# Performance work log

Measured on AMD Instinct MI355X. Metric: run time of the kernel, lower is better.

The kernel has to match this reference:

```python
import jax, jax.numpy as jnp
import numpy as np


def phi(x):
    # ELU + 1 feature map (Katharopoulos et al. 2020)
    return jax.nn.elu(x) + 1.0


def setup_inputs() -> dict:
    key = jax.random.key(0)
    k1, k2, k3 = jax.random.split(key, 3)
    B, T, D = 2, 2048, 512
    x = jax.random.normal(k1, (B, T, D), dtype=jnp.float32)
    # torch nn.Linear stores weight as (out_features, in_features)
    w_qkv = jax.random.normal(k2, (3 * D, D), dtype=jnp.float32) * 0.02
    w_out = jax.random.normal(k3, (D, D), dtype=jnp.float32) * 0.02
    return {"x": x, "w_qkv": w_qkv, "w_out": w_out, "n_heads": 16}


def reference(x, w_qkv, w_out, n_heads):
    B, T, D = x.shape
    H = n_heads
    Dh = D // H
    qkv = x @ w_qkv.T                                   # (B,T,3D)
    qkv = qkv.reshape(B, T, 3, H, Dh).transpose(2, 0, 3, 1, 4)  # (3,B,H,T,Dh)
    q, k, v = phi(qkv[0]), phi(qkv[1]), qkv[2]
    # kv outer product: (B,H,T,Dh_k,Dh_v), causal cumsum over time
    kv = k[..., :, None] * v[..., None, :]
    kv_cumsum = jnp.cumsum(kv, axis=2)
    num = jnp.einsum('bhtd,bhtde->bhte', q, kv_cumsum)  # (B,H,T,Dh)
    k_cumsum = jnp.cumsum(k, axis=2)
    denom = jnp.einsum('bhtd,bhtd->bht', q, k_cumsum)[..., None]
    denom = jnp.maximum(denom, 1e-6)
    out = num / denom                                   # (B,H,T,Dh)
    out = out.transpose(0, 2, 1, 3).reshape(B, T, D)
    return out @ w_out.T
```

## Files before the change

kernel.cpp:

```cpp
#include <hip/hip_runtime.h>
#include <hip/hip_bf16.h>
#include <math.h>

#define B_ 2
#define T_ 2048
#define D_ 512
#define H_ 16
#define DH 32
#define L_ 64
#define C_ 32
#define NC 1024
#define VTP 72
#define CSZ 1056

typedef __attribute__((ext_vector_type(8))) short bf16x8;
typedef __attribute__((ext_vector_type(4))) float f32x4;
typedef __attribute__((ext_vector_type(4))) unsigned short u16x4;

#define AS1 __attribute__((address_space(1)))
#define AS3 __attribute__((address_space(3)))

__device__ __forceinline__ float bf2f(unsigned short u) {
    union { float f; unsigned int i; } v; v.i = ((unsigned int)u) << 16; return v.f;
}
__device__ __forceinline__ unsigned short f2bf(float f) {
    union { float f; unsigned int u; } v; v.f = f;
    unsigned int u = v.u;
    unsigned int r = u + 0x7FFFu + ((u >> 16) & 1u);
    return (unsigned short)(r >> 16);
}
__device__ __forceinline__ unsigned short f2bf_rne(float f) {
    __hip_bfloat16 h = __float2bfloat16(f);
    union { __hip_bfloat16 h; unsigned short u; } v; v.h = h; return v.u;
}
__device__ __forceinline__ bf16x8 phi_frag(bf16x8 in) {
    bf16x8 r;
    #pragma unroll
    for (int i = 0; i < 8; ++i) {
        float f = bf2f((unsigned short)in[i]);
        f = f > 0.f ? f + 1.f : __expf(f);
        r[i] = (short)f2bf(f);
    }
    return r;
}
__device__ __forceinline__ void gload_lds16(const unsigned short* g, unsigned short* l) {
    __builtin_amdgcn_global_load_lds((const AS1 unsigned int*)g, (AS3 unsigned int*)l, 16, 0, 0);
}

template<int BM, bool AF32, bool OUT_BF16>
__global__ __launch_bounds__(256) void gemm_nt(const void* __restrict__ Aptr,
                                               const float* __restrict__ Wf,
                                               void* __restrict__ Cout,
                                               int N, int K)
{
    constexpr int MF = BM / 32;
    constexpr int AF4 = BM / 32;
    __shared__ unsigned short As[2][BM][32];
    __shared__ unsigned short Bs[2][128][32];
    const int tid = threadIdx.x;
    const int lane = tid & 63;
    const int wave = tid >> 6;
    const int wr = wave >> 1;
    const int wc = wave & 1;
    const size_t bm = (size_t)blockIdx.x * BM;
    const size_t bn = (size_t)blockIdx.y * 128;

    const int r8 = lane >> 3;
    const int c4 = (lane & 7) * 4;
    const int lrow = lane >> 2;
    const int lcol = (lane & 3) * 8;

    const float* agf = nullptr;
    const unsigned short* agb = nullptr;
    if constexpr (AF32) agf = (const float*)Aptr + (bm + wave * (BM / 4) + r8) * (size_t)K + c4;
    else                agb = (const unsigned short*)Aptr + (bm + wave * (BM / 4) + lrow) * (size_t)K + lcol;
    const float* wgf = Wf + (bn + wave * 32 + r8) * (size_t)K + c4;

    f32x4 aL[AF4];
    f32x4 wL[4];

    auto load_stage = [&](int buf, int k0) {
        if constexpr (AF32) {
            #pragma unroll
            for (int i = 0; i < AF4; ++i)
                aL[i] = *(const f32x4*)(agf + k0 + (size_t)(i * 8) * K);
        } else {
            gload_lds16(agb + k0, &As[buf][wave * (BM / 4)][0]);
            if constexpr (BM / 4 == 32)
                gload_lds16(agb + (size_t)16 * K + k0, &As[buf][wave * (BM / 4) + 16][0]);
        }
        #pragma unroll
        for (int i = 0; i < 4; ++i)
            wL[i] = *(const f32x4*)(wgf + k0 + (size_t)(i * 8) * K);
    };
    auto write_stage = [&](int buf) {
        if constexpr (AF32) {
            #pragma unroll
            for (int i = 0; i < AF4; ++i) {
                u16x4 o;
                o.x = f2bf_rne(aL[i][0]); o.y = f2bf_rne(aL[i][1]);
                o.z = f2bf_rne(aL[i][2]); o.w = f2bf_rne(aL[i][3]);
                *(u16x4*)&As[buf][wave * (BM / 4) + r8 + i * 8][c4] = o;
            }
        }
        #pragma unroll
        for (int i = 0; i < 4; ++i) {
            u16x4 o;
            o.x = f2bf_rne(wL[i][0]); o.y = f2bf_rne(wL[i][1]);
            o.z = f2bf_rne(wL[i][2]); o.w = f2bf_rne(wL[i][3]);
            *(u16x4*)&Bs[buf][wave * 32 + r8 + i * 8][c4] = o;
        }
    };

    f32x4 acc[MF][4];
    #pragma unroll
    for (int m = 0; m < MF; ++m)
        #pragma unroll
        for (int n = 0; n < 4; ++n)
            acc[m][n] = (f32x4){0.f, 0.f, 0.f, 0.f};

    const int rr = lane & 15;
    const int kb = (lane >> 4) * 8;

    load_stage(0, 0);
    write_stage(0);
    __syncthreads();
    int cur = 0;
    for (int k0 = 0; k0 < K; k0 += 32) {
        const bool more = k0 + 32 < K;
        if (more) load_stage(cur ^ 1, k0 + 32);
        bf16x8 af[MF], bfr[4];
        #pragma unroll
        for (int m = 0; m < MF; ++m)
            af[m] = *(const bf16x8*)&As[cur][wr * (BM / 2) + m * 16 + rr][kb];
        #pragma unroll
        for (int n = 0; n < 4; ++n)
            bfr[n] = *(const bf16x8*)&Bs[cur][wc * 64 + n * 16 + rr][kb];
        #pragma unroll
        for (int m = 0; m < MF; ++m)
            #pragma unroll
            for (int n = 0; n < 4; ++n)
                acc[m][n] = __builtin_amdgcn_mfma_f32_16x16x32_bf16(af[m], bfr[n], acc[m][n], 0, 0, 0);
        if (more) write_stage(cur ^ 1);
        __syncthreads();
        cur ^= 1;
    }

    const int cr = (lane >> 4) * 4;
    const int cc = lane & 15;
    #pragma unroll
    for (int m = 0; m < MF; ++m)
        #pragma unroll
        for (int n = 0; n < 4; ++n)
            #pragma unroll
            for (int j = 0; j < 4; ++j) {
                size_t row = bm + wr * (BM / 2) + m * 16 + cr + j;
                size_t col = bn + wc * 64 + n * 16 + cc;
                float v = acc[m][n][j];
                if (OUT_BF16) ((unsigned short*)Cout)[row * N + col] = f2bf(v);
                else          ((float*)Cout)[row * N + col] = v;
            }
}

__global__ __launch_bounds__(256) void chunk_sum(const unsigned short* __restrict__ qkv,
                                                 float* __restrict__ cSf)
{
    __shared__ unsigned short Kt[4][DH][VTP];
    __shared__ unsigned short Vt[4][48][VTP];
    const int tid = threadIdx.x;
    const int lane = tid & 63;
    const int wave = tid >> 6;
    const int chunk = blockIdx.x * 4 + wave;
    const int c = chunk & 31;
    const int h = (chunk >> 5) & 15;
    const int b = chunk >> 9;
    const size_t rowbase = ((size_t)(b * T_ + c * L_)) * (3 * D_) + h * DH;
    const int half = lane & 1;

    #pragma unroll
    for (int it = 0; it < 2; ++it) {
        int t = (lane >> 1) + it * 32;
        const unsigned short* kp = qkv + rowbase + (size_t)t * (3 * D_) + D_ + half * 16;
        const unsigned short* vp = qkv + rowbase + (size_t)t * (3 * D_) + 2 * D_ + half * 16;
        bf16x8 k0 = phi_frag(*(const bf16x8*)kp);
        bf16x8 k1 = phi_frag(*(const bf16x8*)(kp + 8));
        bf16x8 v0 = *(const bf16x8*)vp;
        bf16x8 v1 = *(const bf16x8*)(vp + 8);
        #pragma unroll
        for (int i = 0; i < 8; ++i) {
            Kt[wave][half * 16 + i][t]     = (unsigned short)k0[i];
            Kt[wave][half * 16 + 8 + i][t] = (unsigned short)k1[i];
            Vt[wave][half * 16 + i][t]     = (unsigned short)v0[i];
            Vt[wave][half * 16 + 8 + i][t] = (unsigned short)v1[i];
        }
    }
    Vt[wave][32][lane] = 0x3F80;

    const int fr = lane & 15;
    const int fg = lane >> 4;
    f32x4 acc[3][2];
    #pragma unroll
    for (int m = 0; m < 3; ++m)
        #pragma unroll
        for (int n = 0; n < 2; ++n)
            acc[m][n] = (f32x4){0.f, 0.f, 0.f, 0.f};

    #pragma unroll
    for (int ks = 0; ks < 2; ++ks) {
        int toff = fg * 8 + ks * 32;
        bf16x8 av[3], bk[2];
        #pragma unroll
        for (int m = 0; m < 3; ++m) av[m] = *(const bf16x8*)&Vt[wave][m * 16 + fr][toff];
        #pragma unroll
        for (int n = 0; n < 2; ++n) bk[n] = *(const bf16x8*)&Kt[wave][n * 16 + fr][toff];
        #pragma unroll
        for (int m = 0; m < 3; ++m)
            #pragma unroll
            for (int n = 0; n < 2; ++n)
                acc[m][n] = __builtin_amdgcn_mfma_f32_16x16x32_bf16(av[m], bk[n], acc[m][n], 0, 0, 0);
    }

    float* outp = cSf + (size_t)chunk * CSZ;
    #pragma unroll
    for (int m = 0; m < 2; ++m)
        #pragma unroll
        for (int n = 0; n < 2; ++n)
            #pragma unroll
            for (int r = 0; r < 4; ++r)
                outp[(m * 16 + fg * 4 + r) * 32 + n * 16 + fr] = acc[m][n][r];
    if (fg == 0) {
        #pragma unroll
        for (int n = 0; n < 2; ++n)
            outp[32 * 32 + n * 16 + fr] = acc[2][n][0];
    }
}

__global__ __launch_bounds__(256) void chunk_scan(const float* __restrict__ cSf,
                                                  unsigned short* __restrict__ cSt)
{
    int idx = blockIdx.x * 256 + threadIdx.x;
    int bh = idx / CSZ;
    int r  = idx % CSZ;
    const float* src = cSf + (size_t)bh * C_ * CSZ + r;
    unsigned short* dst = cSt + (size_t)bh * C_ * CSZ + r;
    float v[C_];
    #pragma unroll
    for (int c = 0; c < C_; ++c) v[c] = src[(size_t)c * CSZ];
    float acc = 0.f;
    #pragma unroll
    for (int c = 0; c < C_; ++c) {
        dst[(size_t)c * CSZ] = f2bf(acc);
        acc += v[c];
    }
}

__global__ __launch_bounds__(256) void chunk_out(const unsigned short* __restrict__ qkv,
                                                 const unsigned short* __restrict__ cSt,
                                                 unsigned short* __restrict__ attn)
{
    __shared__ unsigned short Vt[2][48][VTP];
    __shared__ unsigned short Am[4][32][VTP];
    const int tid = threadIdx.x;
    const int lane = tid & 63;
    const int wave = tid >> 6;
    const int ci = wave >> 1;
    const int wh = wave & 1;
    const int chunk = blockIdx.x * 2 + ci;
    const int c = chunk & 31;
    const int h = (chunk >> 5) & 15;
    const int b = chunk >> 9;
    const size_t rowbase = ((size_t)(b * T_ + c * L_)) * (3 * D_) + h * DH;
    const int fr = lane & 15;
    const int fg = lane >> 4;

    {
        int t = wh * 32 + (lane >> 1);
        int half = lane & 1;
        const unsigned short* vp = qkv + rowbase + (size_t)t * (3 * D_) + 2 * D_ + half * 16;
        bf16x8 v0 = *(const bf16x8*)vp;
        bf16x8 v1 = *(const bf16x8*)(vp + 8);
        #pragma unroll
        for (int i = 0; i < 8; ++i) {
            Vt[ci][half * 16 + i][t]     = (unsigned short)v0[i];
            Vt[ci][half * 16 + 8 + i][t] = (unsigned short)v1[i];
        }
        if (half == 0) Vt[ci][32][t] = 0x3F80;
    }

    bf16x8 aq[2];
    #pragma unroll
    for (int mm = 0; mm < 2; ++mm) {
        int m = wh * 2 + mm;
        const unsigned short* qp = qkv + rowbase + (size_t)(m * 16 + fr) * (3 * D_) + fg * 8;
        aq[mm] = phi_frag(*(const bf16x8*)qp);
    }
    bf16x8 bk[4];
    const int nmax = wh * 2 + 1;
    #pragma unroll
    for (int n = 0; n < 4; ++n) {
        if (n <= nmax) {
            const unsigned short* kp = qkv + rowbase + (size_t)(n * 16 + fr) * (3 * D_) + D_ + fg * 8;
            bk[n] = phi_frag(*(const bf16x8*)kp);
        }
    }
    bf16x8 bkv[3];
    #pragma unroll
    for (int n = 0; n < 3; ++n)
        bkv[n] = *(const bf16x8*)&cSt[(size_t)chunk * CSZ + (size_t)(n * 16 + fr) * 32 + fg * 8];

    f32x4 zero = (f32x4){0.f, 0.f, 0.f, 0.f};
    f32x4 acc[2][3];
    #pragma unroll
    for (int mm = 0; mm < 2; ++mm)
        #pragma unroll
        for (int n = 0; n < 3; ++n)
            acc[mm][n] = __builtin_amdgcn_mfma_f32_16x16x32_bf16(aq[mm], bkv[n], zero, 0, 0, 0);

    #pragma unroll
    for (int mm = 0; mm < 2; ++mm) {
        int m = wh * 2 + mm;
        #pragma unroll
        for (int n = 0; n < 4; ++n) {
            if (n <= m) {
                f32x4 s = __builtin_amdgcn_mfma_f32_16x16x32_bf16(aq[mm], bk[n], zero, 0, 0, 0);
                #pragma unroll
                for (int r = 0; r < 4; ++r) {
                    unsigned short v = f2bf(s[r]);
                    if (n == m && fr > fg * 4 + r) v = 0;
                    Am[wave][mm * 16 + fg * 4 + r][n * 16 + fr] = v;
                }
            }
        }
    }
    {
        int zc = wh ? 48 : 16;
        *(uint2*)&Am[wave][fr][zc + fg * 4] = (uint2){0u, 0u};
    }
    __syncthreads();

    #pragma unroll
    for (int ks = 0; ks < 2; ++ks) {
        if (ks <= wh) {
            bf16x8 bv[3];
            #pragma unroll
            for (int n = 0; n < 3; ++n)
                bv[n] = *(const bf16x8*)&Vt[ci][n * 16 + fr][fg * 8 + ks * 32];
            #pragma unroll
            for (int mm = 0; mm < 2; ++mm) {
                bf16x8 aa = *(const bf16x8*)&Am[wave][mm * 16 + fr][fg * 8 + ks * 32];
                #pragma unroll
                for (int n = 0; n < 3; ++n)
                    acc[mm][n] = __builtin_amdgcn_mfma_f32_16x16x32_bf16(aa, bv[n], acc[mm][n], 0, 0, 0);
            }
        }
    }

    #pragma unroll
    for (int mm = 0; mm < 2; ++mm) {
        float dn[4];
        #pragma unroll
        for (int r = 0; r < 4; ++r)
            dn[r] = __shfl(acc[mm][2][r], lane & 48);
        #pragma unroll
        for (int r = 0; r < 4; ++r) {
            float inv = 1.0f / fmaxf(dn[r], 1e-6f);
            #pragma unroll
            for (int n = 0; n < 2; ++n)
                Am[wave][mm * 16 + fg * 4 + r][n * 16 + fr] = f2bf(acc[mm][n][r] * inv);
        }
    }
    {
        int lrow = lane >> 1;
        int half = lane & 1;
        uint4 q0 = *(const uint4*)&Am[wave][lrow][half * 16];
        uint4 q1 = *(const uint4*)&Am[wave][lrow][half * 16 + 8];
        size_t grow = (size_t)(b * T_ + c * L_ + wh * 32 + lrow);
        unsigned short* dst = attn + grow * D_ + h * DH + half * 16;
        *(uint4*)dst = q0;
        *(uint4*)(dst + 8) = q1;
    }
}

extern "C" void kernel_launch(void* const* d_in, const int* in_sizes, int n_in,
                              void* d_out, int out_size, void* d_ws, size_t ws_size,
                              hipStream_t stream) {
    const float* x     = (const float*)d_in[0];
    const float* w_qkv = (const float*)d_in[1];
    const float* w_out = (const float*)d_in[2];
    float* out = (float*)d_out;

    char* ws = (char*)d_ws;
    unsigned short* qkvb  = (unsigned short*)ws;
    unsigned short* attnb = (unsigned short*)(ws + 12582912);
    float* cSf            = (float*)(ws + 16777216);
    unsigned short* cSt   = (unsigned short*)(ws + 21102592);

    gemm_nt<64, true, true><<<dim3(4096 / 64, 1536 / 128), 256, 0, stream>>>(
        x, w_qkv, qkvb, 1536, 512);

    chunk_sum<<<NC / 4, 256, 0, stream>>>(qkvb, cSf);

    chunk_scan<<<132, 256, 0, stream>>>(cSf, cSt);

    chunk_out<<<NC / 2, 256, 0, stream>>>(qkvb, cSt, attnb);

    gemm_nt<64, false, false><<<dim3(4096 / 64, 512 / 128), 256, 0, stream>>>(
        attnb, w_out, out, 512, 512);
}
```

Measured before the change: 48.60 us.

## Fuse chunk scan into chunk_sum via last-block-done atomic counter

Removes the separate chunk_scan kernel launch by having each chunk_sum block increment a per-(batch,head) atomic counter after writing its chunk sums. The last of the 8 blocks for a given head performs the prefix scan over all 32 chunks and writes the bf16 exclusive prefix states. This saves one launch and the inter-kernel gap, but adds a memset, fences and atomics, and concentrates the scan on only 32 blocks, each using 256 threads for 1056 elements, which may serialize tail work.

Result: slower. 95.81 us (+97.1%).

```diff
diff --git a/kernel.cpp b/kernel.cpp
--- a/kernel.cpp
+++ b/kernel.cpp
@@ -163,10 +163,13 @@
 }
 
 __global__ __launch_bounds__(256) void chunk_sum(const unsigned short* __restrict__ qkv,
-                                                 float* __restrict__ cSf)
+                                                 float* __restrict__ cSf,
+                                                 unsigned short* __restrict__ cSt,
+                                                 unsigned int* __restrict__ cnt)
 {
     __shared__ unsigned short Kt[4][DH][VTP];
     __shared__ unsigned short Vt[4][48][VTP];
+    __shared__ unsigned int slast;
     const int tid = threadIdx.x;
     const int lane = tid & 63;
     const int wave = tid >> 6;
@@ -174,6 +177,7 @@
     const int c = chunk & 31;
     const int h = (chunk >> 5) & 15;
     const int b = chunk >> 9;
+    const int bh = blockIdx.x >> 3;
     const size_t rowbase = ((size_t)(b * T_ + c * L_)) * (3 * D_) + h * DH;
     const int half = lane & 1;
 
@@ -233,24 +237,32 @@
         for (int n = 0; n < 2; ++n)
             outp[32 * 32 + n * 16 + fr] = acc[2][n][0];
     }
-}
-
-__global__ __launch_bounds__(256) void chunk_scan(const float* __restrict__ cSf,
-                                                  unsigned short* __restrict__ cSt)
-{
-    int idx = blockIdx.x * 256 + threadIdx.x;
-    int bh = idx / CSZ;
-    int r  = idx % CSZ;
-    const float* src = cSf + (size_t)bh * C_ * CSZ + r;
-    unsigned short* dst = cSt + (size_t)bh * C_ * CSZ + r;
-    float v[C_];
-    #pragma unroll
-    for (int c = 0; c < C_; ++c) v[c] = src[(size_t)c * CSZ];
-    float acc = 0.f;
-    #pragma unroll
-    for (int c = 0; c < C_; ++c) {
-        dst[(size_t)c * CSZ] = f2bf(acc);
-        acc += v[c];
+
+    __threadfence();
+    __syncthreads();
+    if (tid == 0)
+        slast = (__hip_atomic_fetch_add(&cnt[bh], 1u, __ATOMIC_ACQ_REL,
+                                        __HIP_MEMORY_SCOPE_AGENT) == 7u);
+    __syncthreads();
+    if (slast) {
+        __threadfence();
+        const float* src = cSf + (size_t)bh * C_ * CSZ;
+        unsigned short* dst = cSt + (size_t)bh * C_ * CSZ;
+        #pragma unroll
+        for (int u = 0; u < 5; ++u) {
+            int e = tid + u * 256;
+            if (e < CSZ) {
+                float v[C_];
+                #pragma unroll
+                for (int cc = 0; cc < C_; ++cc) v[cc] = src[(size_t)cc * CSZ + e];
+                float a = 0.f;
+                #pragma unroll
+                for (int cc = 0; cc < C_; ++cc) {
+                    dst[(size_t)cc * CSZ + e] = f2bf(a);
+                    a += v[cc];
+                }
+            }
+        }
     }
 }
 
@@ -394,13 +406,14 @@
     unsigned short* attnb = (unsigned short*)(ws + 12582912);
     float* cSf            = (float*)(ws + 16777216);
     unsigned short* cSt   = (unsigned short*)(ws + 21102592);
+    unsigned int* cnt     = (unsigned int*)(ws + 23265280);
+
+    hipMemsetAsync(cnt, 0, 128, stream);
 
     gemm_nt<64, true, true><<<dim3(4096 / 64, 1536 / 128), 256, 0, stream>>>(
         x, w_qkv, qkvb, 1536, 512);
 
-    chunk_sum<<<NC / 4, 256, 0, stream>>>(qkvb, cSf);
-
-    chunk_scan<<<132, 256, 0, stream>>>(cSf, cSt);
+    chunk_sum<<<NC / 4, 256, 0, stream>>>(qkvb, cSf, cSt, cnt);
 
     chunk_out<<<NC / 2, 256, 0, stream>>>(qkvb, cSt, attnb);
 
```
